# Kernel tuning notes

Hardware: AMD Instinct MI355X
Metric: run time of the kernel (lower is better)

The kernel has to match this reference:

```python
import jax, jax.numpy as jnp
import numpy as np

H, CH = 8, 32            # no_heads, c_hidden
CQ = CK = CV = 128       # input channel dims
B, NR, S = 1, 256, 256   # batch, rows, tokens (Q = K = S)


def setup_inputs() -> dict:
    key = jax.random.key(0)
    ks = jax.random.split(key, 12)
    d = jnp.float32
    inp = {
        "q_x": jax.random.normal(ks[0], (B, NR, S, CQ), d),
        "kv_x": jax.random.normal(ks[1], (B, NR, S, CK), d),
        "bias_mask": jax.random.normal(ks[2], (B, NR, 1, 1, S), d),
        "bias_pair": jax.random.normal(ks[3], (B, 1, H, S, S), d),
        # projection weights stored as [in, out] (math identical to torch W.T)
        "wq": jax.random.normal(ks[4], (CQ, H * CH), d) / np.sqrt(CQ),
        "wk": jax.random.normal(ks[5], (CK, H * CH), d) / np.sqrt(CK),
        "wv": jax.random.normal(ks[6], (CV, H * CH), d) / np.sqrt(CV),
        "wg": jax.random.normal(ks[7], (CQ, H * CH), d) / np.sqrt(CQ),
        "bg": jnp.ones((H * CH,), d),  # gating init: bias = 1
        "wo": jax.random.normal(ks[8], (H * CH, CQ), d) / np.sqrt(H * CH),
        "bo": jnp.zeros((CQ,), d),
    }
    return inp


def _split_heads(y):
    # [..., S, H*CH] -> [..., H, S, CH]
    y = y.reshape(y.shape[:-1] + (H, CH))
    return jnp.swapaxes(y, -2, -3)


def reference(q_x, kv_x, bias_mask, bias_pair, wq, wk, wv, wg, bg, wo, bo):
    scale = 1.0 / np.sqrt(CH).astype(np.float32)
    q = _split_heads(q_x @ wq) * scale          # [B,NR,H,Q,CH]
    k = _split_heads(kv_x @ wk)                 # [B,NR,H,K,CH]
    v = _split_heads(kv_x @ wv)                 # [B,NR,H,K,CH]
    # scores + additive biases (each broadcasts to [B,NR,H,Q,K])
    a = jnp.einsum('...hqc,...hkc->...hqk', q, k) + bias_mask + bias_pair
    a = jax.nn.softmax(a, axis=-1)
    o = jnp.einsum('...hqk,...hkc->...hqc', a, v)  # [B,NR,H,Q,CH]
    o = jnp.swapaxes(o, -2, -3)                    # [B,NR,Q,H,CH]
    # gating from query input
    g = jax.nn.sigmoid(q_x @ wg + bg)
    g = g.reshape(g.shape[:-1] + (H, CH))
    o = o * g
    o = o.reshape(o.shape[:-2] + (H * CH,))
    return o @ wo + bo                              # [B,NR,Q,CQ]
```

## Files before the change

### kernel.cpp

```cpp
#include <hip/hip_runtime.h>
#include <hip/hip_bf16.h>

typedef __bf16 bf16;
typedef __bf16 bf16x8 __attribute__((ext_vector_type(8)));
typedef __bf16 bf16x4 __attribute__((ext_vector_type(4)));
typedef float f32x4 __attribute__((ext_vector_type(4)));


#define M_TOT 65536
#define LOG2E 1.4426950408889634f

static __device__ __forceinline__ f32x4 mfma32(bf16x8 a, bf16x8 b, f32x4 c) {
    return __builtin_amdgcn_mfma_f32_16x16x32_bf16(a, b, c, 0, 0, 0);
}

static __device__ __forceinline__ float exp2_(float x) {
#if __has_builtin(__builtin_amdgcn_exp2f)
    return __builtin_amdgcn_exp2f(x);
#else
    return exp2f(x);
#endif
}

static __device__ __forceinline__ void g2lds16(bf16* lds_base, const bf16* g_lane) {
#if __has_builtin(__builtin_amdgcn_global_load_lds)
    __builtin_amdgcn_global_load_lds(
        (const __attribute__((address_space(1))) void*)g_lane,
        (__attribute__((address_space(3))) void*)lds_base, 16, 0, 0);
#else
    int lane = threadIdx.x & 63;
    *(bf16x8*)(lds_base + lane * 8) = *(const bf16x8*)g_lane;
#endif
}

static __device__ __forceinline__ int permch(int ch) {
    return ((ch >> 2) & 3) * 8 + ((ch >> 4) & 1) * 4 + (ch & 3);
}

__global__ void wprep_kernel(const float* __restrict__ wq, const float* __restrict__ wk,
                             const float* __restrict__ wv, const float* __restrict__ wg,
                             const float* __restrict__ wo, bf16* __restrict__ Wt,
                             const float* __restrict__ bp, bf16* __restrict__ bpb,
                             const float* __restrict__ bm, float* __restrict__ bms)
{
    int job = blockIdx.y;
    int idx = blockIdx.x * 256 + threadIdx.x;
    if (job == 5) {
        for (int i = idx; i < 8 * 256 * 256; i += 32768)
            bpb[i] = (bf16)(bp[i] * LOG2E);
        return;
    }
    if (job == 6) {
        for (int i = idx; i < 65536; i += 32768)
            bms[i] = bm[i] * LOG2E;
        return;
    }
    if (job == 4) {
        int n = idx >> 8, k = idx & 255;
        int h = k >> 5, ch = k & 31;
        Wt[4 * 32768 + n * 256 + h * 32 + permch(ch)] = (bf16)wo[k * 128 + n];
        return;
    }
    const float* src;
    switch (job) {
        case 0: src = wq; break;
        case 1: src = wk; break;
        case 2: src = wv; break;
        default: src = wg; break;
    }
    bf16* dst = Wt + job * 32768;
    int n = idx >> 7, k = idx & 127;
    dst[idx] = (bf16)src[k * 256 + n];
}

template<int MODE1, int MODE2>
static __device__ __forceinline__
void proj_gemm(bf16 (&Xs)[128][136], int mbase, int tid,
               const bf16* __restrict__ WT1, const float* __restrict__ bias1,
               bf16* __restrict__ O1,
               const bf16* __restrict__ WT2, const float* __restrict__ bias2,
               bf16* __restrict__ O2)
{
    const int lane = tid & 63, w = tid >> 6;
    const int c = lane & 15, g = lane >> 4;
    const int nstrip = (w & 3) * 64;
    const int mloc = (w >> 2) * 64;
    const f32x4 fzero = {0.f, 0.f, 0.f, 0.f};

#pragma unroll
    for (int rep = 0; rep < 2; ++rep) {
        const bf16* WT  = rep ? WT2 : WT1;
        const float* bias = rep ? bias2 : bias1;
        bf16* O = rep ? O2 : O1;
        const int MODE = rep ? MODE2 : MODE1;

        f32x4 acc[4][4];
#pragma unroll
        for (int a = 0; a < 4; ++a)
#pragma unroll
            for (int b = 0; b < 4; ++b) acc[a][b] = fzero;

#pragma unroll
        for (int kk = 0; kk < 4; ++kk) {
            bf16x8 af[4], bfr[4];
#pragma unroll
            for (int mi = 0; mi < 4; ++mi)
                af[mi] = *(const bf16x8*)&Xs[mloc + mi * 16 + c][kk * 32 + g * 8];
#pragma unroll
            for (int ni = 0; ni < 4; ++ni)
                bfr[ni] = *(const bf16x8*)(WT + (size_t)(nstrip + ni * 16 + c) * 128 + kk * 32 + g * 8);
#pragma unroll
            for (int mi = 0; mi < 4; ++mi)
#pragma unroll
                for (int ni = 0; ni < 4; ++ni) {
                    if (MODE == 3)
                        acc[mi][ni] = mfma32(af[mi], bfr[ni], acc[mi][ni]);
                    else
                        acc[mi][ni] = mfma32(bfr[ni], af[mi], acc[mi][ni]);
                }
        }

#pragma unroll
        for (int mi = 0; mi < 4; ++mi)
#pragma unroll
            for (int ni = 0; ni < 4; ++ni) {
                if (MODE == 3) {
                    int n = nstrip + ni * 16 + c;
                    int h = n >> 5, ch = n & 31;
                    int m0 = mbase + mloc + mi * 16 + g * 4;
                    int nr = m0 >> 8, t0 = m0 & 255;
                    int tg = t0 >> 2;
                    bf16x4 pk;
#pragma unroll
                    for (int j = 0; j < 4; ++j) pk[j] = (bf16)acc[mi][ni][j];
                    *(bf16x4*)&O[(size_t)(h * 256 + nr) * 8192 + (tg * 32 + (ch ^ (tg & 7))) * 4] = pk;
                } else {
                    int m = mbase + mloc + mi * 16 + c;
                    int n0 = nstrip + ni * 16 + 4 * g;
                    int h = n0 >> 5, ch0 = n0 & 31;
                    if (MODE == 1) {
                        bf16x4 pk;
#pragma unroll
                        for (int j = 0; j < 4; ++j)
                            pk[j] = (bf16)(acc[mi][ni][j] * 0.2550348652402226f);
                        *(bf16x4*)&O[((size_t)h * M_TOT + (size_t)m) * 32 + ch0] = pk;
                    } else if (MODE == 2) {
                        f32x4 b4 = *(const f32x4*)(bias + n0);
                        bf16x4 pk;
#pragma unroll
                        for (int j = 0; j < 4; ++j)
                            pk[j] = (bf16)(1.f / (1.f + __expf(-(acc[mi][ni][j] + b4[j]))));
                        *(bf16x4*)&O[((size_t)h * M_TOT + (size_t)m) * 32 + permch(ch0)] = pk;
                    } else {
                        int nr = m >> 8, t = m & 255;
                        int c4 = ch0 >> 3;
                        bf16x4 pk;
#pragma unroll
                        for (int j = 0; j < 4; ++j) pk[j] = (bf16)acc[mi][ni][j];
                        *(bf16x4*)&O[(size_t)(h * 256 + nr) * 8192 + t * 32 +
                                     ((c4 ^ ((t >> 1) & 3)) << 3) + (ch0 & 7)] = pk;
                    }
                }
            }
    }
}

__global__ __launch_bounds__(512, 2)
void proj_all_kernel(const float* __restrict__ Xq, const float* __restrict__ Xkv,
                     const bf16* __restrict__ Wt, const float* __restrict__ bg,
                     bf16* __restrict__ Q, bf16* __restrict__ G,
                     bf16* __restrict__ Kimg, bf16* __restrict__ Vimg)
{
    __shared__ bf16 Xs[128][136];
    const int which = blockIdx.y;
    const float* X = which ? Xkv : Xq;
    const int tid = threadIdx.x;
    const int mbase = blockIdx.x * 128;

    for (int i = tid; i < 4096; i += 512) {
        int m = i >> 5;
        int k4 = (i & 31) << 2;
        float4 v = *(const float4*)(X + (size_t)(mbase + m) * 128 + k4);
        bf16x4 pk;
        pk.x = (bf16)v.x; pk.y = (bf16)v.y; pk.z = (bf16)v.z; pk.w = (bf16)v.w;
        *(bf16x4*)&Xs[m][k4] = pk;
    }
    __syncthreads();

    if (which == 0)
        proj_gemm<1, 2>(Xs, mbase, tid, Wt, nullptr, Q, Wt + 3 * 32768, bg, G);
    else
        proj_gemm<4, 3>(Xs, mbase, tid, Wt + 1 * 32768, nullptr, Kimg,
                        Wt + 2 * 32768, nullptr, Vimg);
}

__global__ __launch_bounds__(256, 4)
void attn_kernel(const bf16* __restrict__ Q, const bf16* __restrict__ Kimg,
                 const bf16* __restrict__ Vimg, const bf16* __restrict__ G,
                 const float* __restrict__ bms, const bf16* __restrict__ bpb,
                 bf16* __restrict__ Og)
{
    __shared__ bf16 Ks[8192];
    __shared__ bf16 Vs[8192];
    __shared__ float bms_s[256];

    const int h = blockIdx.x, nr = blockIdx.y;
    const int tid = threadIdx.x;
    const int lane = tid & 63, w = tid >> 6;
    const int c = lane & 15, g = lane >> 4;

    const bf16* Kslab = Kimg + (size_t)(h * 256 + nr) * 8192;
    const bf16* Vslab = Vimg + (size_t)(h * 256 + nr) * 8192;
#pragma unroll
    for (int r = 0; r < 4; ++r) {
        int off = (w * 4 + r) * 512;
        g2lds16(&Ks[off], Kslab + off + lane * 8);
        g2lds16(&Vs[off], Vslab + off + lane * 8);
    }
    bms_s[tid] = bms[nr * 256 + tid];
    __syncthreads();

    const bf16* Qh = Q + ((size_t)h * M_TOT + nr * 256) * 32;
    const bf16* Gh = G + ((size_t)h * M_TOT + nr * 256) * 32;
    bf16* Oh = Og + ((size_t)h * M_TOT + nr * 256) * 32;
    const bf16* bph = bpb + (size_t)h * 65536;
    const f32x4 fzero = {0.f, 0.f, 0.f, 0.f};
    const int kswz = (g ^ ((c >> 1) & 3)) << 3;

#pragma unroll
    for (int qc = 0; qc < 4; ++qc) {
        const int q = w * 64 + qc * 16 + c;
        bf16x8 bq = *(const bf16x8*)(Qh + (size_t)q * 32 + g * 8);
        bf16x8 gv8 = *(const bf16x8*)(Gh + (size_t)q * 32 + g * 8);
        const bf16* bpq = bph + (size_t)q * 256;
        bf16x4 bpv[16];
#pragma unroll
        for (int nt = 0; nt < 16; ++nt)
            bpv[nt] = *(const bf16x4*)(bpq + nt * 16 + 4 * g);

        f32x4 s[16];
        __builtin_amdgcn_s_setprio(1);
#pragma unroll
        for (int nt = 0; nt < 16; ++nt) {
            f32x4 cin = *(const f32x4*)&bms_s[nt * 16 + 4 * g];
#pragma unroll
            for (int j = 0; j < 4; ++j) cin[j] += (float)bpv[nt][j];
            bf16x8 ak = *(const bf16x8*)&Ks[(nt * 16 + c) * 32 + kswz];
            s[nt] = mfma32(ak, bq, cin);
        }
        __builtin_amdgcn_s_setprio(0);

        float rs0 = 0.f, rs1 = 0.f, rs2 = 0.f, rs3 = 0.f;
#pragma unroll
        for (int nt = 0; nt < 16; ++nt) {
            float p0 = exp2_(s[nt][0]), p1 = exp2_(s[nt][1]);
            float p2 = exp2_(s[nt][2]), p3 = exp2_(s[nt][3]);
            s[nt][0] = p0; s[nt][1] = p1; s[nt][2] = p2; s[nt][3] = p3;
            rs0 += p0; rs1 += p1; rs2 += p2; rs3 += p3;
        }
        float rs = (rs0 + rs1) + (rs2 + rs3);
        rs += __shfl_xor(rs, 16);
        rs += __shfl_xor(rs, 32);
        float rinv = 1.f / rs;

        f32x4 o[2] = {fzero, fzero};
        __builtin_amdgcn_s_setprio(1);
#pragma unroll
        for (int p2 = 0; p2 < 8; ++p2) {
            bf16x8 pb;
#pragma unroll
            for (int j = 0; j < 4; ++j) {
                pb[j]     = (bf16)s[2 * p2][j];
                pb[4 + j] = (bf16)s[2 * p2 + 1][j];
            }
            const int tg0 = 8 * p2 + g;
            const int tg1 = 8 * p2 + 4 + g;
#pragma unroll
            for (int cc = 0; cc < 2; ++cc) {
                bf16x4 a0 = *(const bf16x4*)&Vs[(tg0 * 32 + ((cc * 16 + c) ^ (tg0 & 7))) * 4];
                bf16x4 a1 = *(const bf16x4*)&Vs[(tg1 * 32 + ((cc * 16 + c) ^ (tg1 & 7))) * 4];
                bf16x8 av = {a0[0], a0[1], a0[2], a0[3], a1[0], a1[1], a1[2], a1[3]};
                o[cc] = mfma32(av, pb, o[cc]);
            }
        }
        __builtin_amdgcn_s_setprio(0);

        bf16x8 ov8;
#pragma unroll
        for (int cc = 0; cc < 2; ++cc)
#pragma unroll
            for (int j = 0; j < 4; ++j)
                ov8[cc * 4 + j] = (bf16)(o[cc][j] * rinv * (float)gv8[cc * 4 + j]);
        *(bf16x8*)(Oh + (size_t)q * 32 + g * 8) = ov8;
    }
}

__global__ __launch_bounds__(256, 4)
void out_proj_kernel(const bf16* __restrict__ Og, const bf16* __restrict__ woT,
                     const float* __restrict__ bo, float* __restrict__ out)
{
    const int tid = threadIdx.x;
    const int lane = tid & 63, w = tid >> 6;
    const int c = lane & 15, g = lane >> 4;
    const int mbase = blockIdx.x * 64;
    const int mstrip = mbase + (w >> 1) * 32;
    const int nstrip = (w & 1) * 64;
    const f32x4 fzero = {0.f, 0.f, 0.f, 0.f};

    f32x4 acc[2][4];
#pragma unroll
    for (int a = 0; a < 2; ++a)
#pragma unroll
        for (int b = 0; b < 4; ++b) acc[a][b] = fzero;

#pragma unroll
    for (int kk = 0; kk < 8; ++kk) {
        bf16x8 af[2], bfr[4];
#pragma unroll
        for (int mi = 0; mi < 2; ++mi)
            af[mi] = *(const bf16x8*)(Og + ((size_t)kk * M_TOT + mstrip + mi * 16 + c) * 32 + g * 8);
#pragma unroll
        for (int ni = 0; ni < 4; ++ni)
            bfr[ni] = *(const bf16x8*)(woT + (size_t)(nstrip + ni * 16 + c) * 256 + kk * 32 + g * 8);
#pragma unroll
        for (int mi = 0; mi < 2; ++mi)
#pragma unroll
            for (int ni = 0; ni < 4; ++ni)
                acc[mi][ni] = mfma32(af[mi], bfr[ni], acc[mi][ni]);
    }

#pragma unroll
    for (int mi = 0; mi < 2; ++mi)
#pragma unroll
        for (int ni = 0; ni < 4; ++ni) {
            int n = nstrip + ni * 16 + c;
            float bias = bo[n];
#pragma unroll
            for (int j = 0; j < 4; ++j) {
                int m = mstrip + mi * 16 + g * 4 + j;
                out[(size_t)m * 128 + n] = acc[mi][ni][j] + bias;
            }
        }
}

extern "C" void kernel_launch(void* const* d_in, const int* in_sizes, int n_in,
                              void* d_out, int out_size, void* d_ws, size_t ws_size,
                              hipStream_t stream)
{
    const float* q_x       = (const float*)d_in[0];
    const float* kv_x      = (const float*)d_in[1];
    const float* bias_mask = (const float*)d_in[2];
    const float* bias_pair = (const float*)d_in[3];
    const float* wq        = (const float*)d_in[4];
    const float* wk        = (const float*)d_in[5];
    const float* wv        = (const float*)d_in[6];
    const float* wg        = (const float*)d_in[7];
    const float* bg        = (const float*)d_in[8];
    const float* wo        = (const float*)d_in[9];
    const float* bo        = (const float*)d_in[10];
    float* out = (float*)d_out;

    char* ws = (char*)d_ws;
    const size_t MB = 1024ull * 1024ull;
    bf16*  Qb  = (bf16*)(ws);
    bf16*  Kb  = (bf16*)(ws + 32 * MB);
    bf16*  Gb  = (bf16*)(ws + 64 * MB);
    bf16*  Vtb = (bf16*)(ws + 96 * MB);
    bf16*  Ogb = (bf16*)(ws + 128 * MB);
    bf16*  Wt  = (bf16*)(ws + 160 * MB);
    bf16*  bpb = (bf16*)(ws + 160 * MB + 512 * 1024);
    float* bms = (float*)(ws + 160 * MB + 2560 * 1024);

    wprep_kernel<<<dim3(128, 7), 256, 0, stream>>>(wq, wk, wv, wg, wo, Wt,
                                                   bias_pair, bpb, bias_mask, bms);

    proj_all_kernel<<<dim3(512, 2), 512, 0, stream>>>(q_x, kv_x, Wt, bg,
                                                      Qb, Gb, Kb, Vtb);

    attn_kernel<<<dim3(8, 256), 256, 0, stream>>>(Qb, Kb, Vtb, Gb, bms, bpb, Ogb);

    out_proj_kernel<<<dim3(1024), 256, 0, stream>>>(Ogb, Wt + 4 * 32768, bo, out);
}
```

Measured before the change: 184.2 us.

## Make attention blocks persistent over four rows with double-buffered K/V prefetch

Each attention block now handles four consecutive rows with 512 threads instead of one row with 256 threads. K, V and mask-bias tiles for the next row are loaded into a second LDS buffer while the current row is computed. The aim is to hide the K/V load latency and cut the number of block launches and prologue syncs. In exchange, LDS per block doubles and the grid shrinks to 512 blocks, which lowers occupancy and parallelism across CUs.

```diff
diff --git a/kernel.cpp b/kernel.cpp
--- a/kernel.cpp
+++ b/kernel.cpp
@@ -194,104 +194,128 @@
                         Wt + 2 * 32768, nullptr, Vimg);
 }
 
-__global__ __launch_bounds__(256, 4)
+__global__ __launch_bounds__(512, 2)
 void attn_kernel(const bf16* __restrict__ Q, const bf16* __restrict__ Kimg,
                  const bf16* __restrict__ Vimg, const bf16* __restrict__ G,
                  const float* __restrict__ bms, const bf16* __restrict__ bpb,
                  bf16* __restrict__ Og)
 {
-    __shared__ bf16 Ks[8192];
-    __shared__ bf16 Vs[8192];
-    __shared__ float bms_s[256];
-
-    const int h = blockIdx.x, nr = blockIdx.y;
+    __shared__ bf16 Ks[2][8192];
+    __shared__ bf16 Vs[2][8192];
+    __shared__ float bms_s[2][256];
+
+    const int h = blockIdx.x;
+    const int nr0 = blockIdx.y * 4;
     const int tid = threadIdx.x;
     const int lane = tid & 63, w = tid >> 6;
     const int c = lane & 15, g = lane >> 4;
-
-    const bf16* Kslab = Kimg + (size_t)(h * 256 + nr) * 8192;
-    const bf16* Vslab = Vimg + (size_t)(h * 256 + nr) * 8192;
-#pragma unroll
-    for (int r = 0; r < 4; ++r) {
-        int off = (w * 4 + r) * 512;
-        g2lds16(&Ks[off], Kslab + off + lane * 8);
-        g2lds16(&Vs[off], Vslab + off + lane * 8);
-    }
-    bms_s[tid] = bms[nr * 256 + tid];
-    __syncthreads();
-
-    const bf16* Qh = Q + ((size_t)h * M_TOT + nr * 256) * 32;
-    const bf16* Gh = G + ((size_t)h * M_TOT + nr * 256) * 32;
-    bf16* Oh = Og + ((size_t)h * M_TOT + nr * 256) * 32;
-    const bf16* bph = bpb + (size_t)h * 65536;
     const f32x4 fzero = {0.f, 0.f, 0.f, 0.f};
     const int kswz = (g ^ ((c >> 1) & 3)) << 3;
-
-#pragma unroll
-    for (int qc = 0; qc < 4; ++qc) {
-        const int q = w * 64 + qc * 16 + c;
-        bf16x8 bq = *(const bf16x8*)(Qh + (size_t)q * 32 + g * 8);
-        bf16x8 gv8 = *(const bf16x8*)(Gh + (size_t)q * 32 + g * 8);
-        const bf16* bpq = bph + (size_t)q * 256;
-        bf16x4 bpv[16];
-#pragma unroll
-        for (int nt = 0; nt < 16; ++nt)
-            bpv[nt] = *(const bf16x4*)(bpq + nt * 16 + 4 * g);
-
-        f32x4 s[16];
-        __builtin_amdgcn_s_setprio(1);
-#pragma unroll
-        for (int nt = 0; nt < 16; ++nt) {
-            f32x4 cin = *(const f32x4*)&bms_s[nt * 16 + 4 * g];
-#pragma unroll
-            for (int j = 0; j < 4; ++j) cin[j] += (float)bpv[nt][j];
-            bf16x8 ak = *(const bf16x8*)&Ks[(nt * 16 + c) * 32 + kswz];
-            s[nt] = mfma32(ak, bq, cin);
+    const bf16* bph = bpb + (size_t)h * 65536;
+
+    {
+        const bf16* Kslab = Kimg + (size_t)(h * 256 + nr0) * 8192;
+        const bf16* Vslab = Vimg + (size_t)(h * 256 + nr0) * 8192;
+#pragma unroll
+        for (int r = 0; r < 2; ++r) {
+            int off = (w * 2 + r) * 512;
+            g2lds16(&Ks[0][off], Kslab + off + lane * 8);
+            g2lds16(&Vs[0][off], Vslab + off + lane * 8);
         }
-        __builtin_amdgcn_s_setprio(0);
-
-        float rs0 = 0.f, rs1 = 0.f, rs2 = 0.f, rs3 = 0.f;
-#pragma unroll
-        for (int nt = 0; nt < 16; ++nt) {
-            float p0 = exp2_(s[nt][0]), p1 = exp2_(s[nt][1]);
-            float p2 = exp2_(s[nt][2]), p3 = exp2_(s[nt][3]);
-            s[nt][0] = p0; s[nt][1] = p1; s[nt][2] = p2; s[nt][3] = p3;
-            rs0 += p0; rs1 += p1; rs2 += p2; rs3 += p3;
+        if (tid < 256) bms_s[0][tid] = bms[nr0 * 256 + tid];
+    }
+    __syncthreads();
+
+#pragma unroll 1
+    for (int it = 0; it < 4; ++it) {
+        const int nr = nr0 + it;
+        const int cur = it & 1;
+
+        if (it < 3) {
+            const int nrn = nr + 1;
+            const bf16* Kslab = Kimg + (size_t)(h * 256 + nrn) * 8192;
+            const bf16* Vslab = Vimg + (size_t)(h * 256 + nrn) * 8192;
+#pragma unroll
+            for (int r = 0; r < 2; ++r) {
+                int off = (w * 2 + r) * 512;
+                g2lds16(&Ks[cur ^ 1][off], Kslab + off + lane * 8);
+                g2lds16(&Vs[cur ^ 1][off], Vslab + off + lane * 8);
+            }
+            if (tid < 256) bms_s[cur ^ 1][tid] = bms[nrn * 256 + tid];
         }
-        float rs = (rs0 + rs1) + (rs2 + rs3);
-        rs += __shfl_xor(rs, 16);
-        rs += __shfl_xor(rs, 32);
-        float rinv = 1.f / rs;
-
-        f32x4 o[2] = {fzero, fzero};
-        __builtin_amdgcn_s_setprio(1);
-#pragma unroll
-        for (int p2 = 0; p2 < 8; ++p2) {
-            bf16x8 pb;
-#pragma unroll
-            for (int j = 0; j < 4; ++j) {
-                pb[j]     = (bf16)s[2 * p2][j];
-                pb[4 + j] = (bf16)s[2 * p2 + 1][j];
-            }
-            const int tg0 = 8 * p2 + g;
-            const int tg1 = 8 * p2 + 4 + g;
-#pragma unroll
-            for (int cc = 0; cc < 2; ++cc) {
-                bf16x4 a0 = *(const bf16x4*)&Vs[(tg0 * 32 + ((cc * 16 + c) ^ (tg0 & 7))) * 4];
-                bf16x4 a1 = *(const bf16x4*)&Vs[(tg1 * 32 + ((cc * 16 + c) ^ (tg1 & 7))) * 4];
-                bf16x8 av = {a0[0], a0[1], a0[2], a0[3], a1[0], a1[1], a1[2], a1[3]};
-                o[cc] = mfma32(av, pb, o[cc]);
-            }
+
+        const bf16* Qh = Q + ((size_t)h * M_TOT + nr * 256) * 32;
+        const bf16* Gh = G + ((size_t)h * M_TOT + nr * 256) * 32;
+        bf16* Oh = Og + ((size_t)h * M_TOT + nr * 256) * 32;
+
+#pragma unroll
+        for (int qc = 0; qc < 2; ++qc) {
+            const int q = w * 32 + qc * 16 + c;
+            bf16x8 bq = *(const bf16x8*)(Qh + (size_t)q * 32 + g * 8);
+            bf16x8 gv8 = *(const bf16x8*)(Gh + (size_t)q * 32 + g * 8);
+            const bf16* bpq = bph + (size_t)q * 256;
+            bf16x4 bpv[16];
+#pragma unroll
+            for (int nt = 0; nt < 16; ++nt)
+                bpv[nt] = *(const bf16x4*)(bpq + nt * 16 + 4 * g);
+
+            f32x4 s[16];
+            __builtin_amdgcn_s_setprio(1);
+#pragma unroll
+            for (int nt = 0; nt < 16; ++nt) {
+                f32x4 cin = *(const f32x4*)&bms_s[cur][nt * 16 + 4 * g];
+#pragma unroll
+                for (int j = 0; j < 4; ++j) cin[j] += (float)bpv[nt][j];
+                bf16x8 ak = *(const bf16x8*)&Ks[cur][(nt * 16 + c) * 32 + kswz];
+                s[nt] = mfma32(ak, bq, cin);
+            }
+            __builtin_amdgcn_s_setprio(0);
+
+            float rs0 = 0.f, rs1 = 0.f, rs2 = 0.f, rs3 = 0.f;
+#pragma unroll
+            for (int nt = 0; nt < 16; ++nt) {
+                float p0 = exp2_(s[nt][0]), p1 = exp2_(s[nt][1]);
+                float p2 = exp2_(s[nt][2]), p3 = exp2_(s[nt][3]);
+                s[nt][0] = p0; s[nt][1] = p1; s[nt][2] = p2; s[nt][3] = p3;
+                rs0 += p0; rs1 += p1; rs2 += p2; rs3 += p3;
+            }
+            float rs = (rs0 + rs1) + (rs2 + rs3);
+            rs += __shfl_xor(rs, 16);
+            rs += __shfl_xor(rs, 32);
+            float rinv = 1.f / rs;
+
+            f32x4 o[2] = {fzero, fzero};
+            __builtin_amdgcn_s_setprio(1);
+#pragma unroll
+            for (int p2 = 0; p2 < 8; ++p2) {
+                bf16x8 pb;
+#pragma unroll
+                for (int j = 0; j < 4; ++j) {
+                    pb[j]     = (bf16)s[2 * p2][j];
+                    pb[4 + j] = (bf16)s[2 * p2 + 1][j];
+                }
+                const int tg0 = 8 * p2 + g;
+                const int tg1 = 8 * p2 + 4 + g;
+#pragma unroll
+                for (int cc = 0; cc < 2; ++cc) {
+                    bf16x4 a0 = *(const bf16x4*)&Vs[cur][(tg0 * 32 + ((cc * 16 + c) ^ (tg0 & 7))) * 4];
+                    bf16x4 a1 = *(const bf16x4*)&Vs[cur][(tg1 * 32 + ((cc * 16 + c) ^ (tg1 & 7))) * 4];
+                    bf16x8 av = {a0[0], a0[1], a0[2], a0[3], a1[0], a1[1], a1[2], a1[3]};
+                    o[cc] = mfma32(av, pb, o[cc]);
+                }
+            }
+            __builtin_amdgcn_s_setprio(0);
+
+            bf16x8 ov8;
+#pragma unroll
+            for (int cc = 0; cc < 2; ++cc)
+#pragma unroll
+                for (int j = 0; j < 4; ++j)
+                    ov8[cc * 4 + j] = (bf16)(o[cc][j] * rinv * (float)gv8[cc * 4 + j]);
+            *(bf16x8*)(Oh + (size_t)q * 32 + g * 8) = ov8;
         }
-        __builtin_amdgcn_s_setprio(0);
-
-        bf16x8 ov8;
-#pragma unroll
-        for (int cc = 0; cc < 2; ++cc)
-#pragma unroll
-            for (int j = 0; j < 4; ++j)
-                ov8[cc * 4 + j] = (bf16)(o[cc][j] * rinv * (float)gv8[cc * 4 + j]);
-        *(bf16x8*)(Oh + (size_t)q * 32 + g * 8) = ov8;
+
+        if (it < 3) __syncthreads();
     }
 }
 
@@ -377,7 +401,7 @@
     proj_all_kernel<<<dim3(512, 2), 512, 0, stream>>>(q_x, kv_x, Wt, bg,
                                                       Qb, Gb, Kb, Vtb);
 
-    attn_kernel<<<dim3(8, 256), 256, 0, stream>>>(Qb, Kb, Vtb, Gb, bms, bpb, Ogb);
+    attn_kernel<<<dim3(8, 64), 512, 0, stream>>>(Qb, Kb, Vtb, Gb, bms, bpb, Ogb);
 
     out_proj_kernel<<<dim3(1024), 256, 0, stream>>>(Ogb, Wt + 4 * 32768, bo, out);
 }
```

New measurement: 195.5 us. +6.1%, slower.
